# Performance work log

Measured on AMD Instinct MI355X. Metric: run time of the kernel, lower is better.

The kernel has to match this reference:

```python
import jax, jax.numpy as jnp
import numpy as np

WS = 512   # window_size
LB = 1     # look_backward
LF = 1     # look_forward
H = 16     # num_attention_heads
NC = LB + LF + 1  # concatenated windows per query window


def _collect(a, pad_value):
    # a: [B, nw, ws, ...]; gather windows [i-LB, i+LF] for each window i,
    # padding the window axis with pad_value (faithful to collect_windows).
    nw = a.shape[1]
    pads = [(0, 0), (LB, LF)] + [(0, 0)] * (a.ndim - 2)
    ap = jnp.pad(a, pads, constant_values=pad_value)
    idx = jnp.arange(nw)[:, None] + jnp.arange(NC)[None, :]  # [nw, NC]
    g = ap[:, idx]  # [B, nw, NC, ws, ...]
    return g.reshape(g.shape[0], nw, NC * a.shape[2], *a.shape[3:])


def setup_inputs() -> dict:
    key = jax.random.key(0)
    ks = jax.random.split(key, 9)
    B, S, E = 1, 4096, 1024
    x = jax.random.normal(ks[0], (B, S, E), dtype=jnp.float32)
    std = 0.02
    wq = std * jax.random.normal(ks[1], (E, E), dtype=jnp.float32)
    wk = std * jax.random.normal(ks[2], (E, E), dtype=jnp.float32)
    wv = std * jax.random.normal(ks[3], (E, E), dtype=jnp.float32)
    wo = std * jax.random.normal(ks[4], (E, E), dtype=jnp.float32)
    bq = std * jax.random.normal(ks[5], (E,), dtype=jnp.float32)
    bk = std * jax.random.normal(ks[6], (E,), dtype=jnp.float32)
    bv = std * jax.random.normal(ks[7], (E,), dtype=jnp.float32)
    bo = std * jax.random.normal(ks[8], (E,), dtype=jnp.float32)
    return {"x": x, "wq": wq, "bq": bq, "wk": wk, "bk": bk,
            "wv": wv, "bv": bv, "wo": wo, "bo": bo}


def reference(x, wq, bq, wk, bk, wv, bv, wo, bo):
    B, S, E = x.shape
    hd = E // H
    nw = S // WS  # seq_len chosen divisible by window_size

    def proj(w, b):
        y = x @ w.T + b
        return y.reshape(B, S, H, hd).transpose(0, 2, 1, 3).reshape(B * H, S, hd)

    q = proj(wq, bq)
    k = proj(wk, bk)
    v = proj(wv, bv)

    qb = q.reshape(B * H, nw, WS, hd)
    # NOTE: original pads K/V window buffers with value -1 (not zero); pad
    # positions are NOT masked (the `!= -1` clause excludes them) -- replicated.
    kb = _collect(k.reshape(B * H, nw, WS, hd), -1.0)  # [BH, nw, NC*WS, hd]
    vb = _collect(v.reshape(B * H, nw, WS, hd), -1.0)

    t = jnp.arange(S, dtype=jnp.int32).reshape(1, nw, WS)
    ct = _collect(t, -1)  # [1, nw, NC*WS] key positions (-1 for pads)

    # Unscaled QK^T (original applies no 1/sqrt(d)).
    scores = jnp.einsum('bwqd,bwkd->bwqk', qb, kb)  # [BH, nw, WS, NC*WS]

    qi = t.reshape(1, nw, WS, 1)          # query absolute positions
    ctb = ct[:, :, None, :]               # key absolute positions
    over = ((ctb > qi + WS * LF) | (ctb < qi - WS * LB)) & (ctb != -1)
    scores = jnp.where(over, -jnp.inf, scores)

    attn = jax.nn.softmax(scores, axis=-1)
    out = jnp.einsum('bwqk,bwkd->bwqd', attn, vb)  # [BH, nw, WS, hd]
    out = out.reshape(B, H, S, hd).transpose(0, 2, 1, 3).reshape(B, S, E)
    return out @ wo.T + bo
```

## Files before the change

### kernel.cpp

```cpp
#include <hip/hip_runtime.h>
#include <stdint.h>

#define S 4096
#define E 1024
#define NH 16
#define HD 64
#define WSZ 512

typedef _Float16 f16x8 __attribute__((ext_vector_type(8)));
typedef _Float16 f16x4 __attribute__((ext_vector_type(4)));
typedef float f32x4 __attribute__((ext_vector_type(4)));
typedef unsigned short u16;
typedef unsigned int u32;

__device__ __forceinline__ u16 f2h_bits(float f) {
    union { _Float16 h; u16 u; } cv; cv.h = (_Float16)f; return cv.u;
}

__device__ __forceinline__ void gld16(const u16* g, u16* l) {
    __builtin_amdgcn_global_load_lds((const __attribute__((address_space(1))) void*)g,
                                     (__attribute__((address_space(3))) void*)l, 16, 0, 0);
}

struct CvtArgs {
    const float* s[5];
    u16* d[5];
    int n[5];
};
__global__ void cvt5(CvtArgs a) {
    int seg = blockIdx.y;
    const float* __restrict__ s = a.s[seg];
    u16* __restrict__ d = a.d[seg];
    int n = a.n[seg];
    for (int i = (blockIdx.x * 256 + threadIdx.x) * 4; i < n; i += gridDim.x * 1024) {
        float4 f = *(const float4*)&s[i];
        uint2 o;
        o.x = (u32)f2h_bits(f.x) | ((u32)f2h_bits(f.y) << 16);
        o.y = (u32)f2h_bits(f.z) | ((u32)f2h_bits(f.w) << 16);
        *(uint2*)&d[i] = o;
    }
}

template <int MODE>
__global__ __launch_bounds__(256) void gemm_bt(
    const u16* __restrict__ A, const u16* __restrict__ B,
    u16* __restrict__ OutQK, u16* __restrict__ OutVT, float* __restrict__ OutF,
    const float* __restrict__ b0, const float* __restrict__ b1, const float* __restrict__ b2,
    int M, int N, int K) {
    __shared__ __align__(16) u16 As[128 * 32];
    __shared__ __align__(16) u16 Bs[128 * 32];
    const int tid = threadIdx.x;
    const int wid = tid >> 6, lid = tid & 63, quad = lid >> 4, l16 = lid & 15;
    const int wm = wid >> 1, wn = wid & 1;
    const int bm0 = blockIdx.y * 128, bn0 = blockIdx.x * 128;

    f32x4 acc[4][4] = {};
    const int sr = tid >> 2, sc = (tid & 3) * 8;

    for (int k0 = 0; k0 < K; k0 += 32) {
        __syncthreads();
        gld16(&A[(size_t)(bm0 + sr) * K + k0 + sc],      &As[tid * 8]);
        gld16(&A[(size_t)(bm0 + sr + 64) * K + k0 + sc], &As[2048 + tid * 8]);
        gld16(&B[(size_t)(bn0 + sr) * K + k0 + sc],      &Bs[tid * 8]);
        gld16(&B[(size_t)(bn0 + sr + 64) * K + k0 + sc], &Bs[2048 + tid * 8]);
        __syncthreads();
        f16x8 af[4], bf[4];
#pragma unroll
        for (int i = 0; i < 4; ++i) af[i] = *(const f16x8*)&As[(wm * 64 + i * 16 + l16) * 32 + quad * 8];
#pragma unroll
        for (int j = 0; j < 4; ++j) bf[j] = *(const f16x8*)&Bs[(wn * 64 + j * 16 + l16) * 32 + quad * 8];
#pragma unroll
        for (int i = 0; i < 4; ++i)
#pragma unroll
            for (int j = 0; j < 4; ++j)
                acc[i][j] = __builtin_amdgcn_mfma_f32_16x16x32_f16(af[i], bf[j], acc[i][j], 0, 0, 0);
    }

    const bool isV = (MODE == 0) && (bn0 >= 2048);
#pragma unroll
    for (int j = 0; j < 4; ++j) {
        int n = bn0 + wn * 64 + j * 16 + l16;
        float bias;
        if (MODE == 1) bias = b0[n];
        else bias = (n < 1024) ? b0[n] : (n < 2048 ? b1[n - 1024] : b2[n - 2048]);
#pragma unroll
        for (int i = 0; i < 4; ++i) {
            int m0 = bm0 + wm * 64 + i * 16 + quad * 4;
            if (MODE == 1) {
#pragma unroll
                for (int r = 0; r < 4; ++r)
                    OutF[(size_t)(m0 + r) * N + n] = acc[i][j][r] + bias;
            } else if (!isV) {
#pragma unroll
                for (int r = 0; r < 4; ++r)
                    OutQK[(size_t)(m0 + r) * 2048 + n] = f2h_bits(acc[i][j][r] + bias);
            } else {
                u16 h0 = f2h_bits(acc[i][j][0] + bias);
                u16 h1 = f2h_bits(acc[i][j][1] + bias);
                u16 h2 = f2h_bits(acc[i][j][2] + bias);
                u16 h3 = f2h_bits(acc[i][j][3] + bias);
                uint2 pk;
                pk.x = (u32)h0 | ((u32)h1 << 16);
                pk.y = (u32)h2 | ((u32)h3 << 16);
                *(uint2*)&OutVT[(size_t)(n - 2048) * 4096 + m0] = pk;
            }
        }
    }
}

__global__ __launch_bounds__(256) void attn_win(const u16* __restrict__ QK, const u16* __restrict__ VT,
                                                u16* __restrict__ AO) {
    const int qt = blockIdx.x, w = blockIdx.y, h = blockIdx.z;
    const int tid = threadIdx.x, wid = tid >> 6, lid = tid & 63, quad = lid >> 4, l16 = lid & 15;

    __shared__ __align__(16) u16 Ks[2][64 * 32];
    __shared__ __align__(16) u16 Vt[2][64 * 36];

    const int qrow0 = w * WSZ + qt * 128 + wid * 32;
    f16x8 qf[2][2];
#pragma unroll
    for (int mt = 0; mt < 2; ++mt)
#pragma unroll
        for (int ks = 0; ks < 2; ++ks)
            qf[mt][ks] = *(const f16x8*)&QK[(size_t)(qrow0 + mt * 16 + l16) * 2048 + h * 64 + ks * 32 + quad * 8];

    f32x4 oacc[2][4] = {};
    float mrun[2] = {-30000.f, -30000.f};
    float lsum[2] = {0.f, 0.f};

    const int g0base = (w - 1) * WSZ;
    const int rqw = qt * 128 + wid * 32 + l16;
    const u16 NEG1 = 0xBC00;

    for (int c = 0; c < 24; ++c) {
        const int g0 = g0base + c * 64;
        const bool pad_chunk = (g0 < 0) || (g0 >= S);
        const bool band = (c * 64 + 63 >= qt * 128) && (c * 64 <= qt * 128 + 1151);
        if (!(pad_chunk || band)) continue;
        const bool interior = (g0 >= 0) && (g0 + 64 <= S);

        __syncthreads();
        if (interior) {
#pragma unroll
            for (int kh = 0; kh < 2; ++kh) {
                const u16* gp = QK + (size_t)(g0 + wid * 16 + (lid >> 2)) * 2048 + 1024 + h * 64 + kh * 32 + (lid & 3) * 8;
                gld16(gp, &Ks[0][0] + (kh * 4 + wid) * 512 + lid * 8);
            }
            {
                int d = tid >> 2, k0 = (tid & 3) * 16;
                const u16* vg = VT + (size_t)(h * 64 + d) * 4096 + g0 + k0;
                uint4 va = *(const uint4*)vg;
                uint4 vb = *(const uint4*)(vg + 8);
                int kh = k0 >> 5, k32 = k0 & 31;
                u16* vp = &Vt[kh][d * 36 + k32];
                *(uint2*)(vp)      = make_uint2(va.x, va.y);
                *(uint2*)(vp + 4)  = make_uint2(va.z, va.w);
                *(uint2*)(vp + 8)  = make_uint2(vb.x, vb.y);
                *(uint2*)(vp + 12) = make_uint2(vb.z, vb.w);
            }
        } else {
#pragma unroll
            for (int rep = 0; rep < 2; ++rep) {
                int ch = tid + rep * 256;
                int row = ch >> 3, cc = (ch & 7) * 8;
                int gk = g0 + row;
                uint4 val;
                if (gk >= 0 && gk < S) val = *(const uint4*)&QK[(size_t)gk * 2048 + 1024 + h * 64 + cc];
                else { u32 p = ((u32)NEG1 << 16) | NEG1; val = make_uint4(p, p, p, p); }
                *(uint4*)&Ks[cc >> 5][row * 32 + (cc & 31)] = val;
            }
            {
                int d = tid >> 2, k0 = (tid & 3) * 16;
                int kh = k0 >> 5, k32 = k0 & 31;
                const u16* vrow = VT + (size_t)(h * 64 + d) * 4096;
#pragma unroll
                for (int grp = 0; grp < 4; ++grp) {
                    u16 tmp[4];
#pragma unroll
                    for (int j = 0; j < 4; ++j) {
                        int key = g0 + k0 + grp * 4 + j;
                        tmp[j] = (key >= 0 && key < S) ? vrow[key] : NEG1;
                    }
                    *(uint2*)&Vt[kh][d * 36 + k32 + grp * 4] =
                        make_uint2((u32)tmp[0] | ((u32)tmp[1] << 16), (u32)tmp[2] | ((u32)tmp[3] << 16));
                }
            }
        }
        __syncthreads();

        f16x8 kf[4][2];
#pragma unroll
        for (int nt = 0; nt < 4; ++nt) {
            kf[nt][0] = *(const f16x8*)&Ks[0][(nt * 16 + l16) * 32 + quad * 8];
            kf[nt][1] = *(const f16x8*)&Ks[1][(nt * 16 + l16) * 32 + quad * 8];
        }
        f16x4 vf[4][4];
#pragma unroll
        for (int dt = 0; dt < 4; ++dt)
#pragma unroll
            for (int nt = 0; nt < 4; ++nt)
                vf[dt][nt] = *(const f16x4*)&Vt[nt >> 1][(dt * 16 + l16) * 36 + (nt & 1) * 16 + quad * 4];

#pragma unroll
        for (int mt = 0; mt < 2; ++mt) {
            f32x4 sc[4];
#pragma unroll
            for (int nt = 0; nt < 4; ++nt) {
                f32x4 t = {};
                t = __builtin_amdgcn_mfma_f32_16x16x32_f16(kf[nt][0], qf[mt][0], t, 0, 0, 0);
                t = __builtin_amdgcn_mfma_f32_16x16x32_f16(kf[nt][1], qf[mt][1], t, 0, 0, 0);
                sc[nt] = t;
            }
            const int rqm = rqw + mt * 16;
            float mloc = mrun[mt];
#pragma unroll
            for (int nt = 0; nt < 4; ++nt)
#pragma unroll
                for (int r = 0; r < 4; ++r) {
                    int n = c * 64 + nt * 16 + quad * 4 + r;
                    int gkey = g0base + n;
                    bool real = ((unsigned)gkey < (unsigned)S);
                    bool masked = real && (n < rqm || n > rqm + 1024);
                    if (masked) sc[nt][r] = -30000.f;
                    mloc = fmaxf(mloc, sc[nt][r]);
                }
            mloc = fmaxf(mloc, __shfl_xor(mloc, 16, 64));
            mloc = fmaxf(mloc, __shfl_xor(mloc, 32, 64));
            float alpha = __expf(mrun[mt] - mloc);
            mrun[mt] = mloc;
            float ls = 0.f;
            f16x4 pf[4];
#pragma unroll
            for (int nt = 0; nt < 4; ++nt)
#pragma unroll
                for (int r = 0; r < 4; ++r) {
                    float p = __expf(sc[nt][r] - mloc);
                    ls += p;
                    pf[nt][r] = (_Float16)p;
                }
            lsum[mt] = lsum[mt] * alpha + ls;
            float ao[4];
#pragma unroll
            for (int r = 0; r < 4; ++r) ao[r] = __shfl(alpha, quad * 4 + r, 64);
#pragma unroll
            for (int dt = 0; dt < 4; ++dt)
#pragma unroll
                for (int r = 0; r < 4; ++r) oacc[mt][dt][r] *= ao[r];
#pragma unroll
            for (int nt = 0; nt < 4; ++nt)
#pragma unroll
                for (int dt = 0; dt < 4; ++dt)
                    oacc[mt][dt] = __builtin_amdgcn_mfma_f32_16x16x16f16(pf[nt], vf[dt][nt], oacc[mt][dt], 0, 0, 0);
        }
    }

#pragma unroll
    for (int mt = 0; mt < 2; ++mt) {
        float lt = lsum[mt];
        lt += __shfl_xor(lt, 16, 64);
        lt += __shfl_xor(lt, 32, 64);
        float linv = 1.f / lt;
        float lrec[4];
#pragma unroll
        for (int r = 0; r < 4; ++r) lrec[r] = __shfl(linv, quad * 4 + r, 64);
#pragma unroll
        for (int dt = 0; dt < 4; ++dt)
#pragma unroll
            for (int r = 0; r < 4; ++r) {
                int srow = w * WSZ + qt * 128 + wid * 32 + mt * 16 + quad * 4 + r;
                int col = h * 64 + dt * 16 + l16;
                AO[(size_t)srow * E + col] = f2h_bits(oacc[mt][dt][r] * lrec[r]);
            }
    }
}

extern "C" void kernel_launch(void* const* d_in, const int* in_sizes, int n_in,
                              void* d_out, int out_size, void* d_ws, size_t ws_size,
                              hipStream_t stream) {
    const float* x  = (const float*)d_in[0];
    const float* wq = (const float*)d_in[1];
    const float* bq = (const float*)d_in[2];
    const float* wk = (const float*)d_in[3];
    const float* bk = (const float*)d_in[4];
    const float* wv = (const float*)d_in[5];
    const float* bv = (const float*)d_in[6];
    const float* wo = (const float*)d_in[7];
    const float* bo = (const float*)d_in[8];
    float* out = (float*)d_out;

    char* ws = (char*)d_ws;
    u16* XH  = (u16*)(ws);
    u16* WC  = (u16*)(ws + 8388608);
    u16* WOh = (u16*)(ws + 14680064);
    u16* QK  = (u16*)(ws + 16777216);
    u16* VTg = (u16*)(ws + 33554432);
    u16* AOh = (u16*)(ws + 41943040);

    CvtArgs ca;
    ca.s[0] = x;  ca.d[0] = XH;            ca.n[0] = 4194304;
    ca.s[1] = wq; ca.d[1] = WC;            ca.n[1] = 1048576;
    ca.s[2] = wk; ca.d[2] = WC + 1048576;  ca.n[2] = 1048576;
    ca.s[3] = wv; ca.d[3] = WC + 2097152;  ca.n[3] = 1048576;
    ca.s[4] = wo; ca.d[4] = WOh;           ca.n[4] = 1048576;
    cvt5<<<dim3(1024, 5), 256, 0, stream>>>(ca);

    gemm_bt<0><<<dim3(24, 32), 256, 0, stream>>>(XH, WC, QK, VTg, nullptr, bq, bk, bv, 4096, 3072, 1024);
    attn_win<<<dim3(4, 8, 16), 256, 0, stream>>>(QK, VTg, AOh);
    gemm_bt<1><<<dim3(8, 32), 256, 0, stream>>>(AOh, WOh, nullptr, nullptr, out, bo, bo, bo, 4096, 1024, 1024);
}
```

Measured before the change: 232.8 us.

## Use 512-thread attention blocks with 16 rows per wave; 64-wide output GEMM tiles

The attention kernel now launches 512 threads per block, with each wave owning 16 query rows instead of 32. This halves per-wave register state and spreads the K/V chunk staging across more threads. It also skips masking for chunks that lie fully inside the band and replaces per-element padding with constant fills. The output projection moves to a dedicated GEMM with 128x64 tiles, doubling its block count so it fills more CUs. In exchange, each K/V chunk is reused by fewer rows per wave, and the larger blocks add synchronisation cost.

```diff
diff --git a/kernel.cpp b/kernel.cpp
--- a/kernel.cpp
+++ b/kernel.cpp
@@ -41,12 +41,11 @@
     }
 }
 
-template <int MODE>
-__global__ __launch_bounds__(256) void gemm_bt(
+__global__ __launch_bounds__(256) void gemm_qkv(
     const u16* __restrict__ A, const u16* __restrict__ B,
-    u16* __restrict__ OutQK, u16* __restrict__ OutVT, float* __restrict__ OutF,
+    u16* __restrict__ OutQK, u16* __restrict__ OutVT,
     const float* __restrict__ b0, const float* __restrict__ b1, const float* __restrict__ b2,
-    int M, int N, int K) {
+    int K) {
     __shared__ __align__(16) u16 As[128 * 32];
     __shared__ __align__(16) u16 Bs[128 * 32];
     const int tid = threadIdx.x;
@@ -76,21 +75,15 @@
                 acc[i][j] = __builtin_amdgcn_mfma_f32_16x16x32_f16(af[i], bf[j], acc[i][j], 0, 0, 0);
     }
 
-    const bool isV = (MODE == 0) && (bn0 >= 2048);
+    const bool isV = (bn0 >= 2048);
 #pragma unroll
     for (int j = 0; j < 4; ++j) {
         int n = bn0 + wn * 64 + j * 16 + l16;
-        float bias;
-        if (MODE == 1) bias = b0[n];
-        else bias = (n < 1024) ? b0[n] : (n < 2048 ? b1[n - 1024] : b2[n - 2048]);
+        float bias = (n < 1024) ? b0[n] : (n < 2048 ? b1[n - 1024] : b2[n - 2048]);
 #pragma unroll
         for (int i = 0; i < 4; ++i) {
             int m0 = bm0 + wm * 64 + i * 16 + quad * 4;
-            if (MODE == 1) {
-#pragma unroll
-                for (int r = 0; r < 4; ++r)
-                    OutF[(size_t)(m0 + r) * N + n] = acc[i][j][r] + bias;
-            } else if (!isV) {
+            if (!isV) {
 #pragma unroll
                 for (int r = 0; r < 4; ++r)
                     OutQK[(size_t)(m0 + r) * 2048 + n] = f2h_bits(acc[i][j][r] + bias);
@@ -108,170 +101,179 @@
     }
 }
 
-__global__ __launch_bounds__(256) void attn_win(const u16* __restrict__ QK, const u16* __restrict__ VT,
-                                                u16* __restrict__ AO) {
+__global__ __launch_bounds__(256) void gemm_n64(
+    const u16* __restrict__ A, const u16* __restrict__ B, float* __restrict__ OutF,
+    const float* __restrict__ bias, int N, int K) {
+    __shared__ __align__(16) u16 As[128 * 32];
+    __shared__ __align__(16) u16 Bs[64 * 32];
+    const int tid = threadIdx.x;
+    const int wid = tid >> 6, lid = tid & 63, quad = lid >> 4, l16 = lid & 15;
+    const int bm0 = blockIdx.y * 128, bn0 = blockIdx.x * 64;
+
+    f32x4 acc[2][4] = {};
+    const int sr = tid >> 2, sc = (tid & 3) * 8;
+
+    for (int k0 = 0; k0 < K; k0 += 32) {
+        __syncthreads();
+        gld16(&A[(size_t)(bm0 + sr) * K + k0 + sc],      &As[tid * 8]);
+        gld16(&A[(size_t)(bm0 + sr + 64) * K + k0 + sc], &As[2048 + tid * 8]);
+        gld16(&B[(size_t)(bn0 + sr) * K + k0 + sc],      &Bs[tid * 8]);
+        __syncthreads();
+        f16x8 af[2], bf[4];
+#pragma unroll
+        for (int i = 0; i < 2; ++i) af[i] = *(const f16x8*)&As[(wid * 32 + i * 16 + l16) * 32 + quad * 8];
+#pragma unroll
+        for (int j = 0; j < 4; ++j) bf[j] = *(const f16x8*)&Bs[(j * 16 + l16) * 32 + quad * 8];
+#pragma unroll
+        for (int i = 0; i < 2; ++i)
+#pragma unroll
+            for (int j = 0; j < 4; ++j)
+                acc[i][j] = __builtin_amdgcn_mfma_f32_16x16x32_f16(af[i], bf[j], acc[i][j], 0, 0, 0);
+    }
+
+#pragma unroll
+    for (int j = 0; j < 4; ++j) {
+        int n = bn0 + j * 16 + l16;
+        float bv = bias[n];
+#pragma unroll
+        for (int i = 0; i < 2; ++i) {
+            int m0 = bm0 + wid * 32 + i * 16 + quad * 4;
+#pragma unroll
+            for (int r = 0; r < 4; ++r)
+                OutF[(size_t)(m0 + r) * N + n] = acc[i][j][r] + bv;
+        }
+    }
+}
+
+__global__ __launch_bounds__(512, 4) void attn_win(const u16* __restrict__ QK, const u16* __restrict__ VT,
+                                                   u16* __restrict__ AO) {
     const int qt = blockIdx.x, w = blockIdx.y, h = blockIdx.z;
     const int tid = threadIdx.x, wid = tid >> 6, lid = tid & 63, quad = lid >> 4, l16 = lid & 15;
 
     __shared__ __align__(16) u16 Ks[2][64 * 32];
     __shared__ __align__(16) u16 Vt[2][64 * 36];
 
-    const int qrow0 = w * WSZ + qt * 128 + wid * 32;
-    f16x8 qf[2][2];
-#pragma unroll
-    for (int mt = 0; mt < 2; ++mt)
-#pragma unroll
-        for (int ks = 0; ks < 2; ++ks)
-            qf[mt][ks] = *(const f16x8*)&QK[(size_t)(qrow0 + mt * 16 + l16) * 2048 + h * 64 + ks * 32 + quad * 8];
-
-    f32x4 oacc[2][4] = {};
-    float mrun[2] = {-30000.f, -30000.f};
-    float lsum[2] = {0.f, 0.f};
+    const int qrow = w * WSZ + qt * 128 + wid * 16 + l16;
+    f16x8 qf[2];
+#pragma unroll
+    for (int ks = 0; ks < 2; ++ks)
+        qf[ks] = *(const f16x8*)&QK[(size_t)qrow * 2048 + h * 64 + ks * 32 + quad * 8];
+
+    f32x4 oacc[4] = {};
+    float mrun = -30000.f;
+    float lsum = 0.f;
 
     const int g0base = (w - 1) * WSZ;
-    const int rqw = qt * 128 + wid * 32 + l16;
+    const int rqloc = qt * 128 + wid * 16 + l16;
+    const int rqw0 = qt * 128 + wid * 16;
     const u16 NEG1 = 0xBC00;
+
+    const int kst = tid & 255, kkh = tid >> 8;
+    const int vd = tid >> 3, vk0 = (tid & 7) * 8;
 
     for (int c = 0; c < 24; ++c) {
         const int g0 = g0base + c * 64;
         const bool pad_chunk = (g0 < 0) || (g0 >= S);
         const bool band = (c * 64 + 63 >= qt * 128) && (c * 64 <= qt * 128 + 1151);
         if (!(pad_chunk || band)) continue;
-        const bool interior = (g0 >= 0) && (g0 + 64 <= S);
-
-        __syncthreads();
-        if (interior) {
-#pragma unroll
-            for (int kh = 0; kh < 2; ++kh) {
-                const u16* gp = QK + (size_t)(g0 + wid * 16 + (lid >> 2)) * 2048 + 1024 + h * 64 + kh * 32 + (lid & 3) * 8;
-                gld16(gp, &Ks[0][0] + (kh * 4 + wid) * 512 + lid * 8);
-            }
+
+        __syncthreads();
+        if (!pad_chunk) {
+            gld16(QK + (size_t)(g0 + (kst >> 2)) * 2048 + 1024 + h * 64 + kkh * 32 + (kst & 3) * 8,
+                  &Ks[0][0] + kkh * 2048 + kst * 8);
             {
-                int d = tid >> 2, k0 = (tid & 3) * 16;
-                const u16* vg = VT + (size_t)(h * 64 + d) * 4096 + g0 + k0;
-                uint4 va = *(const uint4*)vg;
-                uint4 vb = *(const uint4*)(vg + 8);
-                int kh = k0 >> 5, k32 = k0 & 31;
-                u16* vp = &Vt[kh][d * 36 + k32];
-                *(uint2*)(vp)      = make_uint2(va.x, va.y);
-                *(uint2*)(vp + 4)  = make_uint2(va.z, va.w);
-                *(uint2*)(vp + 8)  = make_uint2(vb.x, vb.y);
-                *(uint2*)(vp + 12) = make_uint2(vb.z, vb.w);
+                uint4 va = *(const uint4*)(VT + (size_t)(h * 64 + vd) * 4096 + g0 + vk0);
+                u16* vp = &Vt[vk0 >> 5][vd * 36 + (vk0 & 31)];
+                *(uint2*)(vp)     = make_uint2(va.x, va.y);
+                *(uint2*)(vp + 4) = make_uint2(va.z, va.w);
             }
         } else {
-#pragma unroll
-            for (int rep = 0; rep < 2; ++rep) {
-                int ch = tid + rep * 256;
-                int row = ch >> 3, cc = (ch & 7) * 8;
-                int gk = g0 + row;
-                uint4 val;
-                if (gk >= 0 && gk < S) val = *(const uint4*)&QK[(size_t)gk * 2048 + 1024 + h * 64 + cc];
-                else { u32 p = ((u32)NEG1 << 16) | NEG1; val = make_uint4(p, p, p, p); }
-                *(uint4*)&Ks[cc >> 5][row * 32 + (cc & 31)] = val;
-            }
             {
-                int d = tid >> 2, k0 = (tid & 3) * 16;
-                int kh = k0 >> 5, k32 = k0 & 31;
-                const u16* vrow = VT + (size_t)(h * 64 + d) * 4096;
-#pragma unroll
-                for (int grp = 0; grp < 4; ++grp) {
-                    u16 tmp[4];
-#pragma unroll
-                    for (int j = 0; j < 4; ++j) {
-                        int key = g0 + k0 + grp * 4 + j;
-                        tmp[j] = (key >= 0 && key < S) ? vrow[key] : NEG1;
-                    }
-                    *(uint2*)&Vt[kh][d * 36 + k32 + grp * 4] =
-                        make_uint2((u32)tmp[0] | ((u32)tmp[1] << 16), (u32)tmp[2] | ((u32)tmp[3] << 16));
-                }
-            }
-        }
-        __syncthreads();
-
-        f16x8 kf[4][2];
+                u32 p = ((u32)NEG1 << 16) | NEG1;
+                uint4 val = make_uint4(p, p, p, p);
+                *(uint4*)&Ks[kkh][(kst >> 2) * 32 + (kst & 3) * 8] = val;
+                u16* vp = &Vt[vk0 >> 5][vd * 36 + (vk0 & 31)];
+                *(uint2*)(vp)     = make_uint2(p, p);
+                *(uint2*)(vp + 4) = make_uint2(p, p);
+            }
+        }
+        __syncthreads();
+
+        f32x4 sc[4];
 #pragma unroll
         for (int nt = 0; nt < 4; ++nt) {
-            kf[nt][0] = *(const f16x8*)&Ks[0][(nt * 16 + l16) * 32 + quad * 8];
-            kf[nt][1] = *(const f16x8*)&Ks[1][(nt * 16 + l16) * 32 + quad * 8];
-        }
-        f16x4 vf[4][4];
-#pragma unroll
-        for (int dt = 0; dt < 4; ++dt)
-#pragma unroll
-            for (int nt = 0; nt < 4; ++nt)
-                vf[dt][nt] = *(const f16x4*)&Vt[nt >> 1][(dt * 16 + l16) * 36 + (nt & 1) * 16 + quad * 4];
-
-#pragma unroll
-        for (int mt = 0; mt < 2; ++mt) {
-            f32x4 sc[4];
-#pragma unroll
-            for (int nt = 0; nt < 4; ++nt) {
-                f32x4 t = {};
-                t = __builtin_amdgcn_mfma_f32_16x16x32_f16(kf[nt][0], qf[mt][0], t, 0, 0, 0);
-                t = __builtin_amdgcn_mfma_f32_16x16x32_f16(kf[nt][1], qf[mt][1], t, 0, 0, 0);
-                sc[nt] = t;
-            }
-            const int rqm = rqw + mt * 16;
-            float mloc = mrun[mt];
+            f16x8 kf0 = *(const f16x8*)&Ks[0][(nt * 16 + l16) * 32 + quad * 8];
+            f16x8 kf1 = *(const f16x8*)&Ks[1][(nt * 16 + l16) * 32 + quad * 8];
+            f32x4 t = {};
+            t = __builtin_amdgcn_mfma_f32_16x16x32_f16(kf0, qf[0], t, 0, 0, 0);
+            t = __builtin_amdgcn_mfma_f32_16x16x32_f16(kf1, qf[1], t, 0, 0, 0);
+            sc[nt] = t;
+        }
+
+        const bool needs_mask = !pad_chunk &&
+            ((c * 64 < rqw0 + 16) || (c * 64 + 63 > rqw0 + 1024));
+        if (needs_mask) {
 #pragma unroll
             for (int nt = 0; nt < 4; ++nt)
 #pragma unroll
                 for (int r = 0; r < 4; ++r) {
                     int n = c * 64 + nt * 16 + quad * 4 + r;
-                    int gkey = g0base + n;
-                    bool real = ((unsigned)gkey < (unsigned)S);
-                    bool masked = real && (n < rqm || n > rqm + 1024);
-                    if (masked) sc[nt][r] = -30000.f;
-                    mloc = fmaxf(mloc, sc[nt][r]);
+                    if (n < rqloc || n > rqloc + 1024) sc[nt][r] = -30000.f;
                 }
-            mloc = fmaxf(mloc, __shfl_xor(mloc, 16, 64));
-            mloc = fmaxf(mloc, __shfl_xor(mloc, 32, 64));
-            float alpha = __expf(mrun[mt] - mloc);
-            mrun[mt] = mloc;
-            float ls = 0.f;
-            f16x4 pf[4];
-#pragma unroll
-            for (int nt = 0; nt < 4; ++nt)
-#pragma unroll
-                for (int r = 0; r < 4; ++r) {
-                    float p = __expf(sc[nt][r] - mloc);
-                    ls += p;
-                    pf[nt][r] = (_Float16)p;
-                }
-            lsum[mt] = lsum[mt] * alpha + ls;
-            float ao[4];
-#pragma unroll
-            for (int r = 0; r < 4; ++r) ao[r] = __shfl(alpha, quad * 4 + r, 64);
-#pragma unroll
-            for (int dt = 0; dt < 4; ++dt)
-#pragma unroll
-                for (int r = 0; r < 4; ++r) oacc[mt][dt][r] *= ao[r];
-#pragma unroll
-            for (int nt = 0; nt < 4; ++nt)
-#pragma unroll
-                for (int dt = 0; dt < 4; ++dt)
-                    oacc[mt][dt] = __builtin_amdgcn_mfma_f32_16x16x16f16(pf[nt], vf[dt][nt], oacc[mt][dt], 0, 0, 0);
-        }
-    }
-
-#pragma unroll
-    for (int mt = 0; mt < 2; ++mt) {
-        float lt = lsum[mt];
-        lt += __shfl_xor(lt, 16, 64);
-        lt += __shfl_xor(lt, 32, 64);
-        float linv = 1.f / lt;
-        float lrec[4];
-#pragma unroll
-        for (int r = 0; r < 4; ++r) lrec[r] = __shfl(linv, quad * 4 + r, 64);
+        }
+
+        float mloc = mrun;
+#pragma unroll
+        for (int nt = 0; nt < 4; ++nt) {
+            mloc = fmaxf(mloc, fmaxf(fmaxf(sc[nt][0], sc[nt][1]), fmaxf(sc[nt][2], sc[nt][3])));
+        }
+        mloc = fmaxf(mloc, __shfl_xor(mloc, 16, 64));
+        mloc = fmaxf(mloc, __shfl_xor(mloc, 32, 64));
+        float alpha = __expf(mrun - mloc);
+        mrun = mloc;
+        float ls = 0.f;
+        f16x4 pf[4];
+#pragma unroll
+        for (int nt = 0; nt < 4; ++nt)
+#pragma unroll
+            for (int r = 0; r < 4; ++r) {
+                float p = __expf(sc[nt][r] - mloc);
+                ls += p;
+                pf[nt][r] = (_Float16)p;
+            }
+        lsum = lsum * alpha + ls;
+        float ao[4];
+#pragma unroll
+        for (int r = 0; r < 4; ++r) ao[r] = __shfl(alpha, quad * 4 + r, 64);
 #pragma unroll
         for (int dt = 0; dt < 4; ++dt)
 #pragma unroll
-            for (int r = 0; r < 4; ++r) {
-                int srow = w * WSZ + qt * 128 + wid * 32 + mt * 16 + quad * 4 + r;
-                int col = h * 64 + dt * 16 + l16;
-                AO[(size_t)srow * E + col] = f2h_bits(oacc[mt][dt][r] * lrec[r]);
-            }
-    }
+            for (int r = 0; r < 4; ++r) oacc[dt][r] *= ao[r];
+
+#pragma unroll
+        for (int nt = 0; nt < 4; ++nt)
+#pragma unroll
+            for (int dt = 0; dt < 4; ++dt) {
+                f16x4 vf = *(const f16x4*)&Vt[nt >> 1][(dt * 16 + l16) * 36 + (nt & 1) * 16 + quad * 4];
+                oacc[dt] = __builtin_amdgcn_mfma_f32_16x16x16f16(pf[nt], vf, oacc[dt], 0, 0, 0);
+            }
+    }
+
+    float lt = lsum;
+    lt += __shfl_xor(lt, 16, 64);
+    lt += __shfl_xor(lt, 32, 64);
+    float linv = 1.f / lt;
+    float lrec[4];
+#pragma unroll
+    for (int r = 0; r < 4; ++r) lrec[r] = __shfl(linv, quad * 4 + r, 64);
+#pragma unroll
+    for (int dt = 0; dt < 4; ++dt)
+#pragma unroll
+        for (int r = 0; r < 4; ++r) {
+            int srow = w * WSZ + qt * 128 + wid * 16 + quad * 4 + r;
+            int col = h * 64 + dt * 16 + l16;
+            AO[(size_t)srow * E + col] = f2h_bits(oacc[dt][r] * lrec[r]);
+        }
 }
 
 extern "C" void kernel_launch(void* const* d_in, const int* in_sizes, int n_in,
@@ -304,7 +306,7 @@
     ca.s[4] = wo; ca.d[4] = WOh;           ca.n[4] = 1048576;
     cvt5<<<dim3(1024, 5), 256, 0, stream>>>(ca);
 
-    gemm_bt<0><<<dim3(24, 32), 256, 0, stream>>>(XH, WC, QK, VTg, nullptr, bq, bk, bv, 4096, 3072, 1024);
-    attn_win<<<dim3(4, 8, 16), 256, 0, stream>>>(QK, VTg, AOh);
-    gemm_bt<1><<<dim3(8, 32), 256, 0, stream>>>(AOh, WOh, nullptr, nullptr, out, bo, bo, bo, 4096, 1024, 1024);
-}
+    gemm_qkv<<<dim3(24, 32), 256, 0, stream>>>(XH, WC, QK, VTg, bq, bk, bv, 1024);
+    attn_win<<<dim3(4, 8, 16), 512, 0, stream>>>(QK, VTg, AOh);
+    gemm_n64<<<dim3(16, 32), 256, 0, stream>>>(AOh, WOh, out, bo, 1024, 1024);
+}
```

Measured after the change: 202.0 us. 13.2% less time.
